# Optimization experiments

Hardware: AMD Instinct MI355X
Metric: run time of the kernel (lower is better)

Reference implementation:

```python
import jax, jax.numpy as jnp
import numpy as np

N = 100000
E = 1600000
H = 128            # hidden_dim
ED = 32            # edge_emb_dim
NUM_EDGE_LABELS = 256
NUM_NODE_LABELS = 4096
L = 3              # num_layers
TWO48 = float(2 ** 48 - 1)


def setup_inputs() -> dict:
    key = jax.random.key(0)
    ks = jax.random.split(key, 24)
    s = 0.05
    inp = {
        # hashed scalar node IDs (stored as float32, exactly representable < 2^24)
        "node_features": jax.random.randint(ks[0], (N, 1), 0, 16777215).astype(jnp.float32),
        "edge_index": jax.random.randint(ks[1], (2, E), 0, N, dtype=jnp.int32),
        "edge_attr": jax.random.randint(ks[2], (E,), 0, NUM_EDGE_LABELS, dtype=jnp.int32),
        # input projection + refine
        "W_in": jax.random.normal(ks[3], (1, H), jnp.float32) * s,
        "b_in": jnp.zeros((H,), jnp.float32),
        "W_ref": jax.random.normal(ks[4], (H, H), jnp.float32) * s,
        "b_ref": jnp.zeros((H,), jnp.float32),
        # embedding tables
        "node_emb": jax.random.normal(ks[5], (NUM_NODE_LABELS, H), jnp.float32) * s,
        "edge_emb_tab": jax.random.normal(ks[6], (NUM_EDGE_LABELS, ED), jnp.float32) * s,
        # edge_proj: Linear(ED,ED) -> ReLU -> Linear(ED,ED)
        "Pe1": jax.random.normal(ks[7], (ED, ED), jnp.float32) * s,
        "be1": jnp.zeros((ED,), jnp.float32),
        "Pe2": jax.random.normal(ks[8], (ED, ED), jnp.float32) * s,
        "be2": jnp.zeros((ED,), jnp.float32),
        # per-layer GINEConv params (stacked over layers)
        "W_lin": jax.random.normal(ks[9], (L, ED, H), jnp.float32) * s,   # edge_dim -> hidden
        "b_lin": jnp.zeros((L, H), jnp.float32),
        "W_a": jax.random.normal(ks[10], (L, H, H), jnp.float32) * s,     # mlp layer 1
        "b_a": jnp.zeros((L, H), jnp.float32),
        "W_b": jax.random.normal(ks[11], (L, H, H), jnp.float32) * s,     # mlp layer 2
        "b_b": jnp.zeros((L, H), jnp.float32),
    }
    return inp


def reference(node_features, edge_index, edge_attr,
              W_in, b_in, W_ref, b_ref, node_emb, edge_emb_tab,
              Pe1, be1, Pe2, be2, W_lin, b_lin, W_a, b_a, W_b, b_b):
    n = node_features.shape[0]
    # _prepare_node_features: HASHED, values > 1 -> scale by 2^48-1 and clamp
    x = jnp.clip(node_features / TWO48, 0.0, 1.0)          # [N, 1]
    h = x @ W_in + b_in                                     # input_proj
    h = jax.nn.relu(h) @ W_ref + b_ref                      # input_proj_refine
    # node label embedding: remainder of raw scalar id
    ids = jnp.mod(jax.lax.stop_gradient(node_features[:, 0]).astype(jnp.int32),
                  NUM_NODE_LABELS)
    h = h + node_emb[ids]
    # edge features (identical every layer: shared embedding + proj)
    e = edge_emb_tab[edge_attr]                             # [E, ED]
    e = jax.nn.relu(e @ Pe1 + be1) @ Pe2 + be2              # edge_proj
    src, dst = edge_index[0], edge_index[1]                 # j -> i
    for l in range(L):
        el = e @ W_lin[l] + b_lin[l]                        # GINE lin(edge) -> hidden
        msg = jax.nn.relu(h[src] + el)                      # [E, H]
        agg = jax.ops.segment_sum(msg, dst, num_segments=n) # scatter-add to targets
        z = h + agg                                         # (1+eps)*x + aggr, eps=0
        z = jax.nn.relu(z @ W_a[l] + b_a[l]) @ W_b[l] + b_b[l]
        h = jax.nn.relu(z)                                  # encoder's outer relu
    return h
```

## Files before the change

### kernel.cpp

```cpp
#include <hip/hip_runtime.h>

#define H 128
#define ED 32
#define NLBL 256
#define NNODE_LBL 4096
#define LAYERS 3
#define SPAN 128
#define MAXB 1024
#define ELROWS (NLBL + 1)

typedef short bf16x8 __attribute__((ext_vector_type(8)));
typedef float f32x4 __attribute__((ext_vector_type(4)));
typedef float f32x2 __attribute__((ext_vector_type(2)));

#define TWO48F 281474976710655.0f

static __device__ __forceinline__ float relu_f(float x) { return fmaxf(x, 0.f); }

static __device__ __forceinline__ unsigned short f2bf(float x) {
    unsigned u = __float_as_uint(x);
    return (unsigned short)((u + 0x7fffu + ((u >> 16) & 1u)) >> 16);
}

static __device__ __forceinline__ float bf2f(short b) {
    return __uint_as_float(((unsigned)(unsigned short)b) << 16);
}


__global__ void split_weights_kernel(const float* __restrict__ W_ref,
                                     const float* __restrict__ W_a,
                                     const float* __restrict__ W_b,
                                     unsigned short* __restrict__ out) {
    int mat = blockIdx.y;
    const float* src = (mat == 0) ? W_ref
                     : (mat <= 3) ? W_a + (size_t)(mat - 1) * H * H
                                  : W_b + (size_t)(mat - 4) * H * H;
    int idx = blockIdx.x * 256 + threadIdx.x;
    int k = idx >> 7, c = idx & 127;
    out[(size_t)mat * H * H + (size_t)c * H + k] = f2bf(src[idx]);
}


__global__ void edge_proj_kernel(const float* __restrict__ emb,
                                 const float* __restrict__ Pe1, const float* __restrict__ be1,
                                 const float* __restrict__ Pe2, const float* __restrict__ be2,
                                 float* __restrict__ e_proj) {
    int a = blockIdx.x, d = threadIdx.x;
    __shared__ float t[ED];
    float acc = be1[d];
    for (int k = 0; k < ED; ++k) acc = fmaf(emb[a * ED + k], Pe1[k * ED + d], acc);
    t[d] = fmaxf(acc, 0.f);
    __syncthreads();
    float acc2 = be2[d];
    for (int k = 0; k < ED; ++k) acc2 = fmaf(t[k], Pe2[k * ED + d], acc2);
    e_proj[a * ED + d] = acc2;
}

__global__ void el_tab_kernel(const float* __restrict__ e_proj,
                              const float* __restrict__ W_lin, const float* __restrict__ b_lin,
                              float* __restrict__ el_tab) {
    int a = blockIdx.x, l = blockIdx.y, k = threadIdx.x;
    if (a == NLBL) {
        el_tab[((size_t)l * ELROWS + a) * H + k] = -1e30f;
        return;
    }
    float acc = b_lin[l * H + k];
    for (int d = 0; d < ED; ++d)
        acc = fmaf(e_proj[a * ED + d], W_lin[(l * ED + d) * H + k], acc);
    el_tab[((size_t)l * ELROWS + a) * H + k] = acc;
}


__global__ __launch_bounds__(256) void bucket_hist_kernel(
    const int* __restrict__ dst, int E, int nb, int* __restrict__ bcnt) {
    __shared__ int lh[MAXB];
    for (int i = threadIdx.x; i < nb; i += 256) lh[i] = 0;
    __syncthreads();
    for (int e = blockIdx.x * 256 + threadIdx.x; e < E; e += gridDim.x * 256)
        atomicAdd(&lh[dst[e] >> 7], 1);
    __syncthreads();
    for (int i = threadIdx.x; i < nb; i += 256)
        if (lh[i]) atomicAdd(&bcnt[i], lh[i]);
}

__global__ void bucket_scan_kernel(const int* __restrict__ bcnt, int nb,
                                   int* __restrict__ bbase, int* __restrict__ gcur) {
    __shared__ int s[MAXB];
    int t = threadIdx.x;
    s[t] = (t < nb) ? (bcnt[t] + 3 * SPAN) : 0;
    __syncthreads();
    for (int off = 1; off < MAXB; off <<= 1) {
        int v = (t >= off) ? s[t - off] : 0;
        __syncthreads();
        s[t] += v;
        __syncthreads();
    }
    if (t < nb) {
        int ex = (t == 0) ? 0 : s[t - 1];
        bbase[t] = ex;
        gcur[t] = ex;
    }
    if (t == nb) bbase[nb] = s[nb - 1];
}

__global__ __launch_bounds__(256) void partition_kernel(
    const int* __restrict__ src, const int* __restrict__ dst,
    const int* __restrict__ attr, int E, int nb,
    int* __restrict__ gcur, unsigned* __restrict__ ebuf) {
    __shared__ int lh[MAXB], gofs[MAXB], lc[MAXB];
    const int t = threadIdx.x;
    const int e0 = blockIdx.x * 4096;
    const int e1 = min(e0 + 4096, E);
    for (int i = t; i < nb; i += 256) { lh[i] = 0; lc[i] = 0; }
    __syncthreads();
    for (int e = e0 + t; e < e1; e += 256) atomicAdd(&lh[dst[e] >> 7], 1);
    __syncthreads();
    for (int i = t; i < nb; i += 256)
        if (lh[i]) gofs[i] = atomicAdd(&gcur[i], lh[i]);
    __syncthreads();
    for (int e = e0 + t; e < e1; e += 256) {
        int d = dst[e];
        int b = d >> 7;
        int slot = gofs[b] + atomicAdd(&lc[b], 1);
        ebuf[slot] = (unsigned)src[e] | ((unsigned)attr[e] << 17) | ((unsigned)(d & 127) << 25);
    }
}

__global__ __launch_bounds__(128) void place_kernel(
    const unsigned* __restrict__ ebuf, const int* __restrict__ bbase,
    const int* __restrict__ gcur, int n,
    int* __restrict__ rowptr, int* __restrict__ rowend, int* __restrict__ sorted) {
    __shared__ int rp[SPAN], lc[SPAN], sc[SPAN];
    const int b = blockIdx.x, t = threadIdx.x;
    const int base = bbase[b], rawend = gcur[b];
    lc[t] = 0;
    __syncthreads();
    for (int e = base + t; e < rawend; e += SPAN)
        atomicAdd(&lc[ebuf[e] >> 25], 1);
    __syncthreads();
    const int cnt = lc[t];
    const int pad = (cnt + 3) & ~3;
    sc[t] = pad;
    __syncthreads();
    for (int off = 1; off < SPAN; off <<= 1) {
        int v = (t >= off) ? sc[t - off] : 0;
        __syncthreads();
        sc[t] += v;
        __syncthreads();
    }
    const int mystart = base + sc[t] - pad;
    rp[t] = mystart;
    lc[t] = 0;
    const int node = b * SPAN + t;
    if (node < n) {
        rowptr[node] = mystart;
        rowend[node] = mystart + pad;
    }
    __syncthreads();
    for (int e = base + t; e < rawend; e += SPAN) {
        unsigned p = ebuf[e];
        int dl = p >> 25;
        int pos = rp[dl] + atomicAdd(&lc[dl], 1);
        sorted[pos] = (int)(p & 0x1FFFFFFu);
    }
    __syncthreads();
    if (node < n)
        for (int pos = mystart + cnt; pos < mystart + pad; ++pos)
            sorted[pos] = (NLBL << 17);
}


struct Ed { uint4 hu; float4 e0, e1; };

static __device__ __forceinline__ Ed ld_edge(
    unsigned p, const unsigned* __restrict__ hB, const float* __restrict__ eB) {
    Ed d;
    d.hu = *(const uint4*)(hB + ((p & 131071u) << 6));
    unsigned ao = (p >> 17) << 7;
    d.e0 = *(const float4*)(eB + ao);
    d.e1 = *(const float4*)(eB + ao + 4);
    return d;
}

static __device__ __forceinline__ void acc_edge(
    const Ed& d, f32x2& a0, f32x2& a1, f32x2& a2, f32x2& a3) {
    const f32x2 zero = {0.f, 0.f};
    f32x2 h, s;
    h[0] = __uint_as_float(d.hu.x << 16); h[1] = __uint_as_float(d.hu.x & 0xffff0000u);
    s = h + (f32x2){d.e0.x, d.e0.y};
    a0 = a0 + __builtin_elementwise_max(s, zero);
    h[0] = __uint_as_float(d.hu.y << 16); h[1] = __uint_as_float(d.hu.y & 0xffff0000u);
    s = h + (f32x2){d.e0.z, d.e0.w};
    a1 = a1 + __builtin_elementwise_max(s, zero);
    h[0] = __uint_as_float(d.hu.z << 16); h[1] = __uint_as_float(d.hu.z & 0xffff0000u);
    s = h + (f32x2){d.e1.x, d.e1.y};
    a2 = a2 + __builtin_elementwise_max(s, zero);
    h[0] = __uint_as_float(d.hu.w << 16); h[1] = __uint_as_float(d.hu.w & 0xffff0000u);
    s = h + (f32x2){d.e1.z, d.e1.w};
    a3 = a3 + __builtin_elementwise_max(s, zero);
}

__global__ __launch_bounds__(256) void gather_kernel(
    const unsigned short* __restrict__ hbf, const int* __restrict__ rowptr,
    const int* __restrict__ rowend, const int* __restrict__ sorted,
    const float* __restrict__ el, int n, unsigned short* __restrict__ z) {
    int wave = threadIdx.x >> 6;
    int lane = threadIdx.x & 63;
    int i = blockIdx.x * 4 + wave;
    if (i >= n) return;
    int beg = rowptr[i], end = rowend[i];
    int gg = lane >> 4, m = lane & 15;
    const unsigned* hB = (const unsigned*)hbf + m * 4;
    const float* eB = el + m * 8;
    f32x2 a0 = {0.f, 0.f}, a1 = a0, a2 = a0, a3 = a0;
    int e = beg;
    for (; e + 16 <= end; e += 16) {
        unsigned p0 = (unsigned)sorted[e + gg];
        unsigned p1 = (unsigned)sorted[e + 4 + gg];
        unsigned p2 = (unsigned)sorted[e + 8 + gg];
        unsigned p3 = (unsigned)sorted[e + 12 + gg];
        Ed d0 = ld_edge(p0, hB, eB);
        Ed d1 = ld_edge(p1, hB, eB);
        Ed d2 = ld_edge(p2, hB, eB);
        Ed d3 = ld_edge(p3, hB, eB);
        acc_edge(d0, a0, a1, a2, a3);
        acc_edge(d1, a0, a1, a2, a3);
        acc_edge(d2, a0, a1, a2, a3);
        acc_edge(d3, a0, a1, a2, a3);
    }
    for (; e < end; e += 4) {
        unsigned p = (unsigned)sorted[e + gg];
        Ed d = ld_edge(p, hB, eB);
        acc_edge(d, a0, a1, a2, a3);
    }
    float r[8];
    r[0] = a0[0]; r[1] = a0[1]; r[2] = a1[0]; r[3] = a1[1];
    r[4] = a2[0]; r[5] = a2[1]; r[6] = a3[0]; r[7] = a3[1];
#pragma unroll
    for (int j = 0; j < 8; ++j) {
        r[j] += __shfl_xor(r[j], 16, 64);
        r[j] += __shfl_xor(r[j], 32, 64);
    }
    if (gg == 0) {
        bf16x8 hv = *(const bf16x8*)(hbf + (unsigned)i * H + m * 8);
        bf16x8 o;
#pragma unroll
        for (int j = 0; j < 8; ++j)
            o[j] = (short)f2bf(bf2f(hv[j]) + r[j]);
        *(bf16x8*)(z + (unsigned)i * H + m * 8) = o;
    }
}


__global__ __launch_bounds__(128) void mlp_mfma_kernel(
    const unsigned short* __restrict__ z,
    const unsigned short* __restrict__ WA, const float* __restrict__ ba,
    const unsigned short* __restrict__ WB, const float* __restrict__ bb,
    int n, unsigned short* __restrict__ hbf, float* __restrict__ hf32) {
    __shared__ short sT[2][32 * H];
    const int t = threadIdx.x;
    const int w = t >> 6, lane = t & 63;
    const int m = lane & 15, g = lane >> 4;
    const int nb = blockIdx.x * 64 + w * 32;

    bf16x8 za[2][4];
#pragma unroll
    for (int rt = 0; rt < 2; ++rt) {
        int row = nb + 16 * rt + m; if (row >= n) row = n - 1;
        const unsigned short* zr = z + (size_t)row * H;
#pragma unroll
        for (int ks = 0; ks < 4; ++ks)
            za[rt][ks] = *(const bf16x8*)(zr + 32 * ks + 8 * g);
    }

#pragma unroll 2
    for (int ct = 0; ct < 8; ++ct) {
        float bias = ba[16 * ct + m];
        f32x4 c1[2];
        c1[0] = (f32x4){bias, bias, bias, bias};
        c1[1] = c1[0];
#pragma unroll
        for (int ks = 0; ks < 4; ++ks) {
            bf16x8 bh = *(const bf16x8*)(WA + (size_t)(16 * ct + m) * H + 32 * ks + 8 * g);
            c1[0] = __builtin_amdgcn_mfma_f32_16x16x32_bf16(za[0][ks], bh, c1[0], 0, 0, 0);
            c1[1] = __builtin_amdgcn_mfma_f32_16x16x32_bf16(za[1][ks], bh, c1[1], 0, 0, 0);
        }
#pragma unroll
        for (int rt = 0; rt < 2; ++rt) {
#pragma unroll
            for (int r = 0; r < 4; ++r) {
                float v = fmaxf(c1[rt][r], 0.f);
                int nl = 16 * rt + 4 * g + r;
                int kk = (16 * ct + m) ^ (8 * (nl & 7));
                sT[w][nl * H + kk] = (short)f2bf(v);
            }
        }
    }

    __syncthreads();

    f32x4 c2[2][8];
#pragma unroll
    for (int ct = 0; ct < 8; ++ct) {
        float bias = bb[16 * ct + m];
        c2[0][ct] = (f32x4){bias, bias, bias, bias};
        c2[1][ct] = c2[0][ct];
    }
#pragma unroll 2
    for (int ks = 0; ks < 4; ++ks) {
        bf16x8 ta[2];
#pragma unroll
        for (int rt = 0; rt < 2; ++rt) {
            int nl = 16 * rt + m;
            int kk = (32 * ks + 8 * g) ^ (8 * (nl & 7));
            ta[rt] = *(const bf16x8*)&sT[w][nl * H + kk];
        }
#pragma unroll
        for (int ct = 0; ct < 8; ++ct) {
            bf16x8 bh = *(const bf16x8*)(WB + (size_t)(16 * ct + m) * H + 32 * ks + 8 * g);
            c2[0][ct] = __builtin_amdgcn_mfma_f32_16x16x32_bf16(ta[0], bh, c2[0][ct], 0, 0, 0);
            c2[1][ct] = __builtin_amdgcn_mfma_f32_16x16x32_bf16(ta[1], bh, c2[1][ct], 0, 0, 0);
        }
    }

    if (hf32) {
#pragma unroll
        for (int rt = 0; rt < 2; ++rt)
#pragma unroll
            for (int r = 0; r < 4; ++r) {
                int node = nb + 16 * rt + 4 * g + r;
                if (node < n) {
                    float* hp = hf32 + (size_t)node * H + m;
#pragma unroll
                    for (int ct = 0; ct < 8; ++ct)
                        hp[16 * ct] = fmaxf(c2[rt][ct][r], 0.f);
                }
            }
    } else {
#pragma unroll
        for (int rt = 0; rt < 2; ++rt)
#pragma unroll
            for (int r = 0; r < 4; ++r) {
                int node = nb + 16 * rt + 4 * g + r;
                if (node < n) {
                    unsigned short* hp = hbf + (size_t)node * H + m;
#pragma unroll
                    for (int ct = 0; ct < 8; ++ct)
                        hp[16 * ct] = f2bf(fmaxf(c2[rt][ct][r], 0.f));
                }
            }
    }
}


__global__ __launch_bounds__(128) void input_proj_mfma_kernel(
    const float* __restrict__ nf,
    const float* __restrict__ W_in, const float* __restrict__ b_in,
    const unsigned short* __restrict__ WR, const float* __restrict__ b_ref,
    const float* __restrict__ node_emb,
    int n, unsigned short* __restrict__ hbf) {
    __shared__ float sx[64];
    __shared__ int sid[64];
    const int t = threadIdx.x;
    const int w = t >> 6, lane = t & 63;
    const int m = lane & 15, g = lane >> 4;
    const int nb0 = blockIdx.x * 64;
    if (t < 64) {
        int node = nb0 + t;
        float xv = (node < n) ? nf[node] : 0.f;
        sx[t] = fminf(fmaxf(xv / TWO48F, 0.f), 1.f);
        sid[t] = ((int)xv) & (NNODE_LBL - 1);
    }
    __syncthreads();
    const int nb = nb0 + w * 32;

    bf16x8 ta[2][4];
#pragma unroll
    for (int rt = 0; rt < 2; ++rt) {
        float xv = sx[w * 32 + 16 * rt + m];
#pragma unroll
        for (int ks = 0; ks < 4; ++ks) {
            float4 w0 = *(const float4*)(W_in + 32 * ks + 8 * g);
            float4 w1 = *(const float4*)(W_in + 32 * ks + 8 * g + 4);
            float4 b0 = *(const float4*)(b_in + 32 * ks + 8 * g);
            float4 b1 = *(const float4*)(b_in + 32 * ks + 8 * g + 4);
            bf16x8 v;
            v[0] = (short)f2bf(relu_f(fmaf(xv, w0.x, b0.x)));
            v[1] = (short)f2bf(relu_f(fmaf(xv, w0.y, b0.y)));
            v[2] = (short)f2bf(relu_f(fmaf(xv, w0.z, b0.z)));
            v[3] = (short)f2bf(relu_f(fmaf(xv, w0.w, b0.w)));
            v[4] = (short)f2bf(relu_f(fmaf(xv, w1.x, b1.x)));
            v[5] = (short)f2bf(relu_f(fmaf(xv, w1.y, b1.y)));
            v[6] = (short)f2bf(relu_f(fmaf(xv, w1.z, b1.z)));
            v[7] = (short)f2bf(relu_f(fmaf(xv, w1.w, b1.w)));
            ta[rt][ks] = v;
        }
    }

    f32x4 c2[2][8];
#pragma unroll
    for (int ct = 0; ct < 8; ++ct) {
        float bias = b_ref[16 * ct + m];
        c2[0][ct] = (f32x4){bias, bias, bias, bias};
        c2[1][ct] = c2[0][ct];
    }
#pragma unroll
    for (int ct = 0; ct < 8; ++ct) {
#pragma unroll
        for (int ks = 0; ks < 4; ++ks) {
            bf16x8 bh = *(const bf16x8*)(WR + (size_t)(16 * ct + m) * H + 32 * ks + 8 * g);
            c2[0][ct] = __builtin_amdgcn_mfma_f32_16x16x32_bf16(ta[0][ks], bh, c2[0][ct], 0, 0, 0);
            c2[1][ct] = __builtin_amdgcn_mfma_f32_16x16x32_bf16(ta[1][ks], bh, c2[1][ct], 0, 0, 0);
        }
    }

#pragma unroll
    for (int rt = 0; rt < 2; ++rt)
#pragma unroll
        for (int r = 0; r < 4; ++r) {
            int node = nb + 16 * rt + 4 * g + r;
            if (node < n) {
                int id = sid[w * 32 + 16 * rt + 4 * g + r];
                const float* ep = node_emb + (size_t)id * H + m;
                unsigned short* hp = hbf + (size_t)node * H + m;
#pragma unroll
                for (int ct = 0; ct < 8; ++ct)
                    hp[16 * ct] = f2bf(c2[rt][ct][r] + ep[16 * ct]);
            }
        }
}


extern "C" void kernel_launch(void* const* d_in, const int* in_sizes, int n_in,
                              void* d_out, int out_size, void* d_ws, size_t ws_size,
                              hipStream_t stream) {
    const float* nf       = (const float*)d_in[0];
    const int*   eidx     = (const int*)d_in[1];
    const int*   eattr    = (const int*)d_in[2];
    const float* W_in     = (const float*)d_in[3];
    const float* b_in     = (const float*)d_in[4];
    const float* W_ref    = (const float*)d_in[5];
    const float* b_ref    = (const float*)d_in[6];
    const float* node_emb = (const float*)d_in[7];
    const float* edge_emb = (const float*)d_in[8];
    const float* Pe1      = (const float*)d_in[9];
    const float* be1      = (const float*)d_in[10];
    const float* Pe2      = (const float*)d_in[11];
    const float* be2      = (const float*)d_in[12];
    const float* W_lin    = (const float*)d_in[13];
    const float* b_lin    = (const float*)d_in[14];
    const float* W_a      = (const float*)d_in[15];
    const float* b_a      = (const float*)d_in[16];
    const float* W_b      = (const float*)d_in[17];
    const float* b_b      = (const float*)d_in[18];

    const int N = in_sizes[0];
    const int E = in_sizes[2];
    const int* src = eidx;
    const int* dst = eidx + E;
    const int nb = (N + SPAN - 1) / SPAN;
    const size_t EPAD = (size_t)E + (size_t)3 * SPAN * nb + 64;

    char* ws = (char*)d_ws;
    size_t off = 0;
    auto carve = [&](size_t bytes) -> void* {
        void* p = (void*)(ws + off);
        off = (off + bytes + 511) & ~(size_t)511;
        return p;
    };
    unsigned short* z      = (unsigned short*)carve((size_t)N * H * sizeof(unsigned short));
    unsigned short* hbf    = (unsigned short*)carve((size_t)N * H * sizeof(unsigned short));
    unsigned* ebuf  = (unsigned*)carve(EPAD * sizeof(unsigned));
    int*   sorted = (int*)carve(EPAD * sizeof(int));
    int*   rowptr = (int*)carve((size_t)(N + 1) * sizeof(int));
    int*   rowend = (int*)carve((size_t)N * sizeof(int));
    int*   bcnt   = (int*)carve((size_t)nb * sizeof(int));
    int*   bbase  = (int*)carve((size_t)(nb + 1) * sizeof(int));
    int*   gcur   = (int*)carve((size_t)nb * sizeof(int));
    float* el_tab = (float*)carve((size_t)LAYERS * ELROWS * H * sizeof(float));
    float* e_proj = (float*)carve((size_t)NLBL * ED * sizeof(float));
    unsigned short* wsp = (unsigned short*)carve((size_t)7 * H * H * sizeof(unsigned short));
    float* h_out = (float*)d_out;

    split_weights_kernel<<<dim3(64, 7), 256, 0, stream>>>(W_ref, W_a, W_b, wsp);

    hipMemsetAsync(bcnt, 0, (size_t)nb * sizeof(int), stream);
    bucket_hist_kernel<<<512, 256, 0, stream>>>(dst, E, nb, bcnt);
    bucket_scan_kernel<<<1, MAXB, 0, stream>>>(bcnt, nb, bbase, gcur);
    partition_kernel<<<(E + 4095) / 4096, 256, 0, stream>>>(src, dst, eattr, E, nb, gcur, ebuf);
    place_kernel<<<nb, SPAN, 0, stream>>>(ebuf, bbase, gcur, N, rowptr, rowend, sorted);

    edge_proj_kernel<<<NLBL, ED, 0, stream>>>(edge_emb, Pe1, be1, Pe2, be2, e_proj);
    el_tab_kernel<<<dim3(ELROWS, LAYERS), H, 0, stream>>>(e_proj, W_lin, b_lin, el_tab);

    const int gridMM = (N + 63) / 64;
    input_proj_mfma_kernel<<<gridMM, 128, 0, stream>>>(
        nf, W_in, b_in, wsp, b_ref, node_emb, N, hbf);

    for (int l = 0; l < LAYERS; ++l) {
        gather_kernel<<<(N + 3) / 4, 256, 0, stream>>>(
            hbf, rowptr, rowend, sorted, el_tab + (size_t)l * ELROWS * H, N, z);
        mlp_mfma_kernel<<<gridMM, 128, 0, stream>>>(
            z,
            wsp + (size_t)(1 + l) * H * H, b_a + (size_t)l * H,
            wsp + (size_t)(4 + l) * H * H, b_b + (size_t)l * H,
            N, hbf, (l == LAYERS - 1) ? h_out : nullptr);
    }
}
```

Baseline: 429.5 us.

## Fuse edge gather and node MLP into one per-layer kernel with ping-pong buffers

Replaces the separate gather and MLP kernels with one layer kernel. Each wave aggregates 16 nodes sequentially into a swizzled LDS tile, then runs both MFMA matmuls on that tile, so the z intermediate never goes to global memory. Because the layer now reads and writes node features in the same kernel, the output goes to a second buffer and the two are swapped each layer. In exchange, each wave walks its 16 nodes serially with a shorter edge unroll, which lowers memory-level parallelism in the gather, and MFMA work per wave drops to one 16-row tile.

```diff
diff --git a/kernel.cpp b/kernel.cpp
--- a/kernel.cpp
+++ b/kernel.cpp
@@ -200,155 +200,125 @@
     a3 = a3 + __builtin_elementwise_max(s, zero);
 }
 
-__global__ __launch_bounds__(256) void gather_kernel(
-    const unsigned short* __restrict__ hbf, const int* __restrict__ rowptr,
-    const int* __restrict__ rowend, const int* __restrict__ sorted,
-    const float* __restrict__ el, int n, unsigned short* __restrict__ z) {
-    int wave = threadIdx.x >> 6;
-    int lane = threadIdx.x & 63;
-    int i = blockIdx.x * 4 + wave;
-    if (i >= n) return;
-    int beg = rowptr[i], end = rowend[i];
-    int gg = lane >> 4, m = lane & 15;
-    const unsigned* hB = (const unsigned*)hbf + m * 4;
-    const float* eB = el + m * 8;
-    f32x2 a0 = {0.f, 0.f}, a1 = a0, a2 = a0, a3 = a0;
-    int e = beg;
-    for (; e + 16 <= end; e += 16) {
-        unsigned p0 = (unsigned)sorted[e + gg];
-        unsigned p1 = (unsigned)sorted[e + 4 + gg];
-        unsigned p2 = (unsigned)sorted[e + 8 + gg];
-        unsigned p3 = (unsigned)sorted[e + 12 + gg];
-        Ed d0 = ld_edge(p0, hB, eB);
-        Ed d1 = ld_edge(p1, hB, eB);
-        Ed d2 = ld_edge(p2, hB, eB);
-        Ed d3 = ld_edge(p3, hB, eB);
-        acc_edge(d0, a0, a1, a2, a3);
-        acc_edge(d1, a0, a1, a2, a3);
-        acc_edge(d2, a0, a1, a2, a3);
-        acc_edge(d3, a0, a1, a2, a3);
-    }
-    for (; e < end; e += 4) {
-        unsigned p = (unsigned)sorted[e + gg];
-        Ed d = ld_edge(p, hB, eB);
-        acc_edge(d, a0, a1, a2, a3);
-    }
-    float r[8];
-    r[0] = a0[0]; r[1] = a0[1]; r[2] = a1[0]; r[3] = a1[1];
-    r[4] = a2[0]; r[5] = a2[1]; r[6] = a3[0]; r[7] = a3[1];
-#pragma unroll
-    for (int j = 0; j < 8; ++j) {
-        r[j] += __shfl_xor(r[j], 16, 64);
-        r[j] += __shfl_xor(r[j], 32, 64);
-    }
-    if (gg == 0) {
-        bf16x8 hv = *(const bf16x8*)(hbf + (unsigned)i * H + m * 8);
-        bf16x8 o;
-#pragma unroll
-        for (int j = 0; j < 8; ++j)
-            o[j] = (short)f2bf(bf2f(hv[j]) + r[j]);
-        *(bf16x8*)(z + (unsigned)i * H + m * 8) = o;
-    }
-}
-
-
-__global__ __launch_bounds__(128) void mlp_mfma_kernel(
-    const unsigned short* __restrict__ z,
+__global__ __launch_bounds__(256) void layer_kernel(
+    const unsigned short* __restrict__ hbf,
+    const int* __restrict__ rowptr, const int* __restrict__ rowend,
+    const int* __restrict__ sorted, const float* __restrict__ el,
     const unsigned short* __restrict__ WA, const float* __restrict__ ba,
     const unsigned short* __restrict__ WB, const float* __restrict__ bb,
-    int n, unsigned short* __restrict__ hbf, float* __restrict__ hf32) {
-    __shared__ short sT[2][32 * H];
+    int n, unsigned short* __restrict__ hout, float* __restrict__ hf32) {
+    __shared__ short zb[4][16 * H];
     const int t = threadIdx.x;
     const int w = t >> 6, lane = t & 63;
     const int m = lane & 15, g = lane >> 4;
-    const int nb = blockIdx.x * 64 + w * 32;
-
-    bf16x8 za[2][4];
-#pragma unroll
-    for (int rt = 0; rt < 2; ++rt) {
-        int row = nb + 16 * rt + m; if (row >= n) row = n - 1;
-        const unsigned short* zr = z + (size_t)row * H;
-#pragma unroll
-        for (int ks = 0; ks < 4; ++ks)
-            za[rt][ks] = *(const bf16x8*)(zr + 32 * ks + 8 * g);
-    }
+    const int nb = blockIdx.x * 64 + w * 16;
+
+    const unsigned* hB = (const unsigned*)hbf + m * 4;
+    const float* eB = el + m * 8;
+#pragma unroll 1
+    for (int nl = 0; nl < 16; ++nl) {
+        const int i = nb + nl;
+        f32x2 a0 = {0.f, 0.f}, a1 = a0, a2 = a0, a3 = a0;
+        if (i < n) {
+            int beg = rowptr[i], end = rowend[i];
+            int e = beg;
+            for (; e + 8 <= end; e += 8) {
+                unsigned pA = (unsigned)sorted[e + g];
+                unsigned pB = (unsigned)sorted[e + 4 + g];
+                Ed dA = ld_edge(pA, hB, eB);
+                Ed dB = ld_edge(pB, hB, eB);
+                acc_edge(dA, a0, a1, a2, a3);
+                acc_edge(dB, a0, a1, a2, a3);
+            }
+            if (e < end) {
+                unsigned p = (unsigned)sorted[e + g];
+                Ed d = ld_edge(p, hB, eB);
+                acc_edge(d, a0, a1, a2, a3);
+            }
+        }
+        float r[8];
+        r[0] = a0[0]; r[1] = a0[1]; r[2] = a1[0]; r[3] = a1[1];
+        r[4] = a2[0]; r[5] = a2[1]; r[6] = a3[0]; r[7] = a3[1];
+#pragma unroll
+        for (int j = 0; j < 8; ++j) {
+            r[j] += __shfl_xor(r[j], 16, 64);
+            r[j] += __shfl_xor(r[j], 32, 64);
+        }
+        if (g == 0) {
+            bf16x8 o;
+            if (i < n) {
+                bf16x8 hv = *(const bf16x8*)(hbf + (unsigned)i * H + m * 8);
+#pragma unroll
+                for (int j = 0; j < 8; ++j)
+                    o[j] = (short)f2bf(bf2f(hv[j]) + r[j]);
+            } else {
+#pragma unroll
+                for (int j = 0; j < 8; ++j) o[j] = 0;
+            }
+            *(bf16x8*)&zb[w][nl * H + ((m * 8) ^ (8 * (nl & 7)))] = o;
+        }
+    }
+
+    bf16x8 za[4];
+#pragma unroll
+    for (int ks = 0; ks < 4; ++ks)
+        za[ks] = *(const bf16x8*)&zb[w][m * H + ((32 * ks + 8 * g) ^ (8 * (m & 7)))];
 
 #pragma unroll 2
     for (int ct = 0; ct < 8; ++ct) {
         float bias = ba[16 * ct + m];
-        f32x4 c1[2];
-        c1[0] = (f32x4){bias, bias, bias, bias};
-        c1[1] = c1[0];
+        f32x4 c1 = (f32x4){bias, bias, bias, bias};
 #pragma unroll
         for (int ks = 0; ks < 4; ++ks) {
             bf16x8 bh = *(const bf16x8*)(WA + (size_t)(16 * ct + m) * H + 32 * ks + 8 * g);
-            c1[0] = __builtin_amdgcn_mfma_f32_16x16x32_bf16(za[0][ks], bh, c1[0], 0, 0, 0);
-            c1[1] = __builtin_amdgcn_mfma_f32_16x16x32_bf16(za[1][ks], bh, c1[1], 0, 0, 0);
-        }
-#pragma unroll
-        for (int rt = 0; rt < 2; ++rt) {
-#pragma unroll
-            for (int r = 0; r < 4; ++r) {
-                float v = fmaxf(c1[rt][r], 0.f);
-                int nl = 16 * rt + 4 * g + r;
-                int kk = (16 * ct + m) ^ (8 * (nl & 7));
-                sT[w][nl * H + kk] = (short)f2bf(v);
-            }
-        }
-    }
-
-    __syncthreads();
-
-    f32x4 c2[2][8];
+            c1 = __builtin_amdgcn_mfma_f32_16x16x32_bf16(za[ks], bh, c1, 0, 0, 0);
+        }
+#pragma unroll
+        for (int r = 0; r < 4; ++r) {
+            float v = fmaxf(c1[r], 0.f);
+            int nl = 4 * g + r;
+            zb[w][nl * H + ((16 * ct + m) ^ (8 * (nl & 7)))] = (short)f2bf(v);
+        }
+    }
+
+    f32x4 c2[8];
 #pragma unroll
     for (int ct = 0; ct < 8; ++ct) {
         float bias = bb[16 * ct + m];
-        c2[0][ct] = (f32x4){bias, bias, bias, bias};
-        c2[1][ct] = c2[0][ct];
+        c2[ct] = (f32x4){bias, bias, bias, bias};
     }
 #pragma unroll 2
     for (int ks = 0; ks < 4; ++ks) {
-        bf16x8 ta[2];
-#pragma unroll
-        for (int rt = 0; rt < 2; ++rt) {
-            int nl = 16 * rt + m;
-            int kk = (32 * ks + 8 * g) ^ (8 * (nl & 7));
-            ta[rt] = *(const bf16x8*)&sT[w][nl * H + kk];
-        }
+        bf16x8 ta = *(const bf16x8*)&zb[w][m * H + ((32 * ks + 8 * g) ^ (8 * (m & 7)))];
 #pragma unroll
         for (int ct = 0; ct < 8; ++ct) {
             bf16x8 bh = *(const bf16x8*)(WB + (size_t)(16 * ct + m) * H + 32 * ks + 8 * g);
-            c2[0][ct] = __builtin_amdgcn_mfma_f32_16x16x32_bf16(ta[0], bh, c2[0][ct], 0, 0, 0);
-            c2[1][ct] = __builtin_amdgcn_mfma_f32_16x16x32_bf16(ta[1], bh, c2[1][ct], 0, 0, 0);
+            c2[ct] = __builtin_amdgcn_mfma_f32_16x16x32_bf16(ta, bh, c2[ct], 0, 0, 0);
         }
     }
 
     if (hf32) {
 #pragma unroll
-        for (int rt = 0; rt < 2; ++rt)
-#pragma unroll
-            for (int r = 0; r < 4; ++r) {
-                int node = nb + 16 * rt + 4 * g + r;
-                if (node < n) {
-                    float* hp = hf32 + (size_t)node * H + m;
-#pragma unroll
-                    for (int ct = 0; ct < 8; ++ct)
-                        hp[16 * ct] = fmaxf(c2[rt][ct][r], 0.f);
-                }
-            }
+        for (int r = 0; r < 4; ++r) {
+            int node = nb + 4 * g + r;
+            if (node < n) {
+                float* hp = hf32 + (size_t)node * H + m;
+#pragma unroll
+                for (int ct = 0; ct < 8; ++ct)
+                    hp[16 * ct] = fmaxf(c2[ct][r], 0.f);
+            }
+        }
     } else {
 #pragma unroll
-        for (int rt = 0; rt < 2; ++rt)
-#pragma unroll
-            for (int r = 0; r < 4; ++r) {
-                int node = nb + 16 * rt + 4 * g + r;
-                if (node < n) {
-                    unsigned short* hp = hbf + (size_t)node * H + m;
-#pragma unroll
-                    for (int ct = 0; ct < 8; ++ct)
-                        hp[16 * ct] = f2bf(fmaxf(c2[rt][ct][r], 0.f));
-                }
-            }
+        for (int r = 0; r < 4; ++r) {
+            int node = nb + 4 * g + r;
+            if (node < n) {
+                unsigned short* hp = hout + (size_t)node * H + m;
+#pragma unroll
+                for (int ct = 0; ct < 8; ++ct)
+                    hp[16 * ct] = f2bf(fmaxf(c2[ct][r], 0.f));
+            }
+        }
     }
 }
 
@@ -468,8 +438,8 @@
         off = (off + bytes + 511) & ~(size_t)511;
         return p;
     };
-    unsigned short* z      = (unsigned short*)carve((size_t)N * H * sizeof(unsigned short));
     unsigned short* hbf    = (unsigned short*)carve((size_t)N * H * sizeof(unsigned short));
+    unsigned short* hbf2   = (unsigned short*)carve((size_t)N * H * sizeof(unsigned short));
     unsigned* ebuf  = (unsigned*)carve(EPAD * sizeof(unsigned));
     int*   sorted = (int*)carve(EPAD * sizeof(int));
     int*   rowptr = (int*)carve((size_t)(N + 1) * sizeof(int));
@@ -493,17 +463,18 @@
     edge_proj_kernel<<<NLBL, ED, 0, stream>>>(edge_emb, Pe1, be1, Pe2, be2, e_proj);
     el_tab_kernel<<<dim3(ELROWS, LAYERS), H, 0, stream>>>(e_proj, W_lin, b_lin, el_tab);
 
-    const int gridMM = (N + 63) / 64;
-    input_proj_mfma_kernel<<<gridMM, 128, 0, stream>>>(
+    input_proj_mfma_kernel<<<(N + 63) / 64, 128, 0, stream>>>(
         nf, W_in, b_in, wsp, b_ref, node_emb, N, hbf);
 
+    const int gridL = (N + 63) / 64;
+    unsigned short* hin = hbf;
+    unsigned short* hnx = hbf2;
     for (int l = 0; l < LAYERS; ++l) {
-        gather_kernel<<<(N + 3) / 4, 256, 0, stream>>>(
-            hbf, rowptr, rowend, sorted, el_tab + (size_t)l * ELROWS * H, N, z);
-        mlp_mfma_kernel<<<gridMM, 128, 0, stream>>>(
-            z,
+        layer_kernel<<<gridL, 256, 0, stream>>>(
+            hin, rowptr, rowend, sorted, el_tab + (size_t)l * ELROWS * H,
             wsp + (size_t)(1 + l) * H * H, b_a + (size_t)l * H,
             wsp + (size_t)(4 + l) * H * H, b_b + (size_t)l * H,
-            N, hbf, (l == LAYERS - 1) ? h_out : nullptr);
-    }
-}
+            N, hnx, (l == LAYERS - 1) ? h_out : nullptr);
+        unsigned short* tmp = hin; hin = hnx; hnx = tmp;
+    }
+}
```

After: 541.5 us. 26.1% more time.
